# Kernel tuning notes

Hardware: AMD Instinct MI355X
Metric: run time of the kernel (lower is better)

The kernel has to match this reference:

```python
import jax, jax.numpy as jnp
import numpy as np

NUM_STEPS = 32
SEQ = 64
IN = 512
HID = 256
NUM_CLASSES = 10
BATCH = 2048


def _lstm_layer(xseq, Wih, Whh, bih, bhh):
    # xseq: (T, B, D). PyTorch LSTMCell gate order: i, f, g, o.
    B = xseq.shape[1]
    H = Whh.shape[1]
    h0 = jnp.zeros((B, H), xseq.dtype)
    c0 = jnp.zeros((B, H), xseq.dtype)
    b = bih + bhh

    def step(carry, x):
        h, c = carry
        gates = x @ Wih.T + h @ Whh.T + b  # (B, 4H)
        i, f, g, o = jnp.split(gates, 4, axis=-1)
        c_new = jax.nn.sigmoid(f) * c + jax.nn.sigmoid(i) * jnp.tanh(g)
        h_new = jax.nn.sigmoid(o) * jnp.tanh(c_new)
        return (h_new, c_new), h_new

    (hT, cT), hs = jax.lax.scan(step, (h0, c0), xseq)
    return hs, hT


def _run_stack(xseq, layer_params):
    hT = None
    for (Wih, Whh, bih, bhh) in layer_params:
        xseq, hT = _lstm_layer(xseq, Wih, Whh, bih, bhh)
    return hT


def setup_inputs() -> dict:
    key = jax.random.key(0)
    ks = jax.random.split(key, 32)
    d = {"xs": jax.random.normal(ks[0], (BATCH, SEQ, IN), dtype=jnp.float32)}
    cfg = [IN, HID, HID]
    ki = 1
    for direc in ("f", "r"):
        for l, (di, dh) in enumerate(zip(cfg[:-1], cfg[1:])):
            s = 1.0 / np.sqrt(dh)
            d[f"Wih_{direc}{l}"] = jax.random.uniform(ks[ki], (4 * dh, di), minval=-s, maxval=s); ki += 1
            d[f"Whh_{direc}{l}"] = jax.random.uniform(ks[ki], (4 * dh, dh), minval=-s, maxval=s); ki += 1
            d[f"bih_{direc}{l}"] = jax.random.uniform(ks[ki], (4 * dh,), minval=-s, maxval=s); ki += 1
            d[f"bhh_{direc}{l}"] = jax.random.uniform(ks[ki], (4 * dh,), minval=-s, maxval=s); ki += 1
    s = 1.0 / np.sqrt(2 * HID)
    d["W3"] = jax.random.uniform(ks[ki], (NUM_CLASSES, 2 * HID), minval=-s, maxval=s); ki += 1
    d["b3"] = jax.random.uniform(ks[ki], (NUM_CLASSES,), minval=-s, maxval=s)
    return d


def reference(xs, Wih_f0, Whh_f0, bih_f0, bhh_f0, Wih_f1, Whh_f1, bih_f1, bhh_f1,
              Wih_r0, Whh_r0, bih_r0, bhh_r0, Wih_r1, Whh_r1, bih_r1, bhh_r1, W3, b3):
    # forward direction: timesteps 62-NUM_STEPS .. 61
    xf = jnp.transpose(xs[:, 62 - NUM_STEPS:62, :], (1, 0, 2))  # (T, B, D)
    hF = _run_stack(xf, [(Wih_f0, Whh_f0, bih_f0, bhh_f0),
                         (Wih_f1, Whh_f1, bih_f1, bhh_f1)])
    # reverse direction: last 3 frames in order 63, 62, 61
    xr = jnp.transpose(jnp.flip(xs[:, 61:64, :], axis=1), (1, 0, 2))  # (3, B, D)
    hR = _run_stack(xr, [(Wih_r0, Whh_r0, bih_r0, bhh_r0),
                         (Wih_r1, Whh_r1, bih_r1, bhh_r1)])
    latent = jnp.concatenate([hF, hR], axis=1)  # (B, 512)
    return latent @ W3.T + b3
```

## Files before the change

### kernel.cpp

```cpp
#include <hip/hip_runtime.h>
#include <stdint.h>

typedef unsigned short u16;
typedef unsigned long long u64;
typedef __attribute__((ext_vector_type(8)))  short  bf16x8;
typedef __attribute__((ext_vector_type(8)))  u16    u16x8;
typedef __attribute__((ext_vector_type(4)))  float  f32x4;
typedef __attribute__((ext_vector_type(16))) _Float16 f16x16;

#define MFMA_BF16(a,b,c) __builtin_amdgcn_mfma_f32_16x16x32_bf16((a),(b),(c),0,0,0)

#define BATCH   2048
#define FSTEPS  32
#define RSTEPS  3
#define NVF     35

static constexpr size_t HROW32 = 128;
static constexpr size_t HPAR32 = (size_t)BATCH * HROW32;

static constexpr size_t OFF_CTL  = 0;
static constexpr size_t OFF_H0G  = 32768;
static constexpr size_t OFF_H1G  = OFF_H0G + HPAR32 * 2 * 4;
static constexpr size_t OFF_LAT  = OFF_H1G + HPAR32 * 2 * 4;
static constexpr size_t OFF_XP   = OFF_LAT + (size_t)BATCH * 512 * 4;
static constexpr size_t XP_BYTES = (size_t)NVF * BATCH * 1024 * 2;
static constexpr size_t OFF_W0XF = OFF_XP + XP_BYTES;
static constexpr size_t OFF_W0XR = OFF_W0XF + (size_t)1024 * 512 * 2;
static constexpr size_t OFF_P0F  = OFF_W0XR + (size_t)1024 * 512 * 2;
static constexpr size_t OFF_P0R  = OFF_P0F + (size_t)32768 * 16;
static constexpr size_t OFF_P1F  = OFF_P0R + (size_t)32768 * 16;
static constexpr size_t OFF_P1R  = OFF_P1F + (size_t)65536 * 16;
static constexpr size_t OFF_BS0F = OFF_P1R + (size_t)65536 * 16;
static constexpr size_t OFF_BS0R = OFF_BS0F + 4096;
static constexpr size_t OFF_BS1F = OFF_BS0R + 4096;
static constexpr size_t OFF_BS1R = OFF_BS1F + 4096;
static constexpr size_t WS_NEED  = OFF_BS1R + 4096;

__device__ __forceinline__ u16 f2bf(float f) {
    unsigned u = __float_as_uint(f);
    unsigned r = (u + 0x7fffu + ((u >> 16) & 1u)) >> 16;
    return (u16)r;
}
__device__ __forceinline__ float sigm(float x) { return 1.0f / (1.0f + __expf(-x)); }
__device__ __forceinline__ float tanh_fast(float x) {
    float a = fabsf(x);
    float e = __expf(-2.0f * a);
    float t = (1.0f - e) / (1.0f + e);
    return x < 0.0f ? -t : t;
}
__device__ __forceinline__ u16 f2h(float f) {
    _Float16 h = (_Float16)f;
    union { _Float16 h; u16 b; } u; u.h = h; return u.b;
}

__device__ __forceinline__ bf16x8 ldsA(const char* H, int row, int k) {
    int byte = (row << 9) + (k << 1);
    byte ^= (row & 7) << 4;
    return *(const bf16x8*)(H + byte);
}

__device__ __forceinline__ void reload32(char* Hs, const u64* src, int rg, int tid) {
    u64 v[8];
#pragma unroll
    for (int i = 0; i < 8; ++i) {
        int idx = tid + (i << 8);
        v[i] = __hip_atomic_load(src + ((size_t)rg * 32 + (idx >> 6)) * 64 + (idx & 63),
                                 __ATOMIC_RELAXED, __HIP_MEMORY_SCOPE_AGENT);
    }
#pragma unroll
    for (int i = 0; i < 8; ++i) {
        int idx = tid + (i << 8);
        int row = idx >> 6, cu = idx & 63;
        int byte = (row << 9) + (cu << 3);
        byte ^= (row & 7) << 4;
        *(u64*)(Hs + byte) = v[i];
    }
}

__global__ void __launch_bounds__(256)
lstm_seq(const _Float16* __restrict__ xp,
         const u16* __restrict__ P0f_, const u16* __restrict__ P0r_,
         const u16* __restrict__ P1f_, const u16* __restrict__ P1r_,
         const float* __restrict__ bs1f, const float* __restrict__ bs1r,
         unsigned* __restrict__ h0g, unsigned* __restrict__ h1g,
         float* __restrict__ latent, unsigned* __restrict__ ctl)
{
    __shared__ char T0[16384];
    __shared__ char T1[16384];
    const int tid = threadIdx.x, wq = tid >> 6, lane = tid & 63;
    const int bid = blockIdx.x;
    const int colq = bid >> 6;
    const int rg   = bid & 63;
    const int mem  = colq * 4 + wq;
    const int hc   = mem * 16 + (lane & 15);
    const int klane = lane >> 4, q4 = klane << 2;
    unsigned* flag = ctl + (size_t)rg * 64;
    unsigned bcount = 0;

    for (int dir = 0; dir < 2; ++dir) {
        const int nst = dir ? RSTEPS : FSTEPS;
        const int gbase = dir ? FSTEPS : 0;
        const bf16x8* P0v = (const bf16x8*)(dir ? P0r_ : P0f_) + (size_t)mem * (8 * 4 * 64);
        const bf16x8* P1v = (const bf16x8*)(dir ? P1r_ : P1f_) + (size_t)mem * (16 * 4 * 64);
        const float* bs1 = dir ? bs1r : bs1f;
        float b1reg[4];
#pragma unroll
        for (int g = 0; g < 4; ++g) b1reg[g] = bs1[g * 256 + hc];

        float c0[2][4], c1[2][4];
#pragma unroll
        for (int Mt = 0; Mt < 2; ++Mt)
#pragma unroll
            for (int r = 0; r < 4; ++r) { c0[Mt][r] = 0.f; c1[Mt][r] = 0.f; }

        __syncthreads();
#pragma unroll
        for (int i = 0; i < 4; ++i) {
            ((f32x4*)T0)[i * 256 + tid] = (f32x4){0.f, 0.f, 0.f, 0.f};
            ((f32x4*)T1)[i * 256 + tid] = (f32x4){0.f, 0.f, 0.f, 0.f};
        }
        __syncthreads();

        f16x16 xqm[2];
#pragma unroll
        for (int Mt = 0; Mt < 2; ++Mt)
            xqm[Mt] = *(const f16x16*)(xp +
                ((((size_t)gbase * 128 + rg * 2 + Mt) * 16 + mem) * 64 + lane) * 16);

        for (int t = 0; t <= nst; ++t) {
            f32x4 acc1[4][2];
            if (t >= 1) {
#pragma unroll
                for (int g = 0; g < 4; ++g) { acc1[g][0] = (f32x4){0.f,0.f,0.f,0.f}; acc1[g][1] = (f32x4){0.f,0.f,0.f,0.f}; }
#pragma unroll
                for (int kc = 0; kc < 8; ++kc) {
                    bf16x8 a0 = ldsA(T0, (lane & 15),       kc * 32 + klane * 8);
                    bf16x8 a1 = ldsA(T0, 16 + (lane & 15),  kc * 32 + klane * 8);
#pragma unroll
                    for (int g = 0; g < 4; ++g) {
                        bf16x8 b = P1v[(kc * 4 + g) * 64 + lane];
                        acc1[g][0] = MFMA_BF16(a0, b, acc1[g][0]);
                        acc1[g][1] = MFMA_BF16(a1, b, acc1[g][1]);
                    }
                }
                if (t >= 2) {
#pragma unroll
                    for (int kc = 0; kc < 8; ++kc) {
                        bf16x8 a0 = ldsA(T1, (lane & 15),      kc * 32 + klane * 8);
                        bf16x8 a1 = ldsA(T1, 16 + (lane & 15), kc * 32 + klane * 8);
#pragma unroll
                        for (int g = 0; g < 4; ++g) {
                            bf16x8 b = P1v[((kc + 8) * 4 + g) * 64 + lane];
                            acc1[g][0] = MFMA_BF16(a0, b, acc1[g][0]);
                            acc1[g][1] = MFMA_BF16(a1, b, acc1[g][1]);
                        }
                    }
                }
            }

            f32x4 acc0[4][2];
            if (t < nst) {
#pragma unroll
                for (int g = 0; g < 4; ++g) { acc0[g][0] = (f32x4){0.f,0.f,0.f,0.f}; acc0[g][1] = (f32x4){0.f,0.f,0.f,0.f}; }
                if (t >= 1) {
#pragma unroll
                    for (int kc = 0; kc < 8; ++kc) {
                        bf16x8 a0 = ldsA(T0, (lane & 15),      kc * 32 + klane * 8);
                        bf16x8 a1 = ldsA(T0, 16 + (lane & 15), kc * 32 + klane * 8);
#pragma unroll
                        for (int g = 0; g < 4; ++g) {
                            bf16x8 b = P0v[(kc * 4 + g) * 64 + lane];
                            acc0[g][0] = MFMA_BF16(a0, b, acc0[g][0]);
                            acc0[g][1] = MFMA_BF16(a1, b, acc0[g][1]);
                        }
                    }
                }
            }

            if (t < nst) {
                unsigned* dst = h0g + (size_t)(t & 1) * HPAR32;
                const int cp = mem * 8 + ((lane & 15) >> 1);
#pragma unroll
                for (int Mt = 0; Mt < 2; ++Mt) {
                    float hn[4];
#pragma unroll
                    for (int r = 0; r < 4; ++r) {
                        float gi = acc0[0][Mt][r] + (float)xqm[Mt][0 * 4 + r];
                        float gf = acc0[1][Mt][r] + (float)xqm[Mt][1 * 4 + r];
                        float gg = acc0[2][Mt][r] + (float)xqm[Mt][2 * 4 + r];
                        float go = acc0[3][Mt][r] + (float)xqm[Mt][3 * 4 + r];
                        float cn = sigm(gf) * c0[Mt][r] + sigm(gi) * tanh_fast(gg);
                        c0[Mt][r] = cn;
                        hn[r] = sigm(go) * tanh_fast(cn);
                    }
                    const int rowbase = rg * 32 + Mt * 16 + q4;
#pragma unroll
                    for (int r = 0; r < 4; ++r) {
                        float p = __shfl_xor(hn[r], 1);
                        if (!(lane & 1)) {
                            unsigned w = (unsigned)f2bf(hn[r]) | ((unsigned)f2bf(p) << 16);
                            __hip_atomic_store(dst + (size_t)(rowbase + r) * HROW32 + cp, w,
                                               __ATOMIC_RELAXED, __HIP_MEMORY_SCOPE_AGENT);
                        }
                    }
                }
            }

            if (t >= 1) {
                const int cp = mem * 8 + ((lane & 15) >> 1);
#pragma unroll
                for (int Mt = 0; Mt < 2; ++Mt) {
                    float hn[4];
#pragma unroll
                    for (int r = 0; r < 4; ++r) {
                        float gi = acc1[0][Mt][r] + b1reg[0];
                        float gf = acc1[1][Mt][r] + b1reg[1];
                        float gg = acc1[2][Mt][r] + b1reg[2];
                        float go = acc1[3][Mt][r] + b1reg[3];
                        float cn = sigm(gf) * c1[Mt][r] + sigm(gi) * tanh_fast(gg);
                        c1[Mt][r] = cn;
                        hn[r] = sigm(go) * tanh_fast(cn);
                    }
                    const int rowbase = rg * 32 + Mt * 16 + q4;
                    if (t < nst) {
                        unsigned* dst = h1g + (size_t)((t - 1) & 1) * HPAR32;
#pragma unroll
                        for (int r = 0; r < 4; ++r) {
                            float p = __shfl_xor(hn[r], 1);
                            if (!(lane & 1)) {
                                unsigned w = (unsigned)f2bf(hn[r]) | ((unsigned)f2bf(p) << 16);
                                __hip_atomic_store(dst + (size_t)(rowbase + r) * HROW32 + cp, w,
                                                   __ATOMIC_RELAXED, __HIP_MEMORY_SCOPE_AGENT);
                            }
                        }
                    } else {
#pragma unroll
                        for (int r = 0; r < 4; ++r)
                            latent[(size_t)(rowbase + r) * 512 + dir * 256 + hc] = hn[r];
                    }
                }
            }

            if (t < nst) {
                ++bcount;
                asm volatile("s_waitcnt vmcnt(0)" ::: "memory");
                __syncthreads();
                if (tid == 0)
                    __hip_atomic_fetch_add(flag, 1u, __ATOMIC_RELAXED, __HIP_MEMORY_SCOPE_AGENT);
                if (t + 1 < nst) {
#pragma unroll
                    for (int Mt = 0; Mt < 2; ++Mt)
                        xqm[Mt] = *(const f16x16*)(xp +
                            ((((size_t)(gbase + t + 1) * 128 + rg * 2 + Mt) * 16 + mem) * 64 + lane) * 16);
                }
                if (tid == 0) {
                    while (__hip_atomic_load(flag, __ATOMIC_RELAXED, __HIP_MEMORY_SCOPE_AGENT)
                           < 4u * bcount) {}
                }
                __syncthreads();
                __builtin_amdgcn_sched_barrier(0);
                reload32(T0, (const u64*)(h0g + (size_t)(t & 1) * HPAR32), rg, tid);
                if (t >= 1)
                    reload32(T1, (const u64*)(h1g + (size_t)((t - 1) & 1) * HPAR32), rg, tid);
                __syncthreads();
            }
        }
    }
}

__global__ void __launch_bounds__(256)
xproj_gemm(const float* __restrict__ xs,
           const u16* __restrict__ W0xf, const u16* __restrict__ W0xr,
           const float* __restrict__ bs0f, const float* __restrict__ bs0r,
           _Float16* __restrict__ xp)
{
    __shared__ char As[16384];
    __shared__ char Bs[16384];
    const int tid = threadIdx.x, wv = tid >> 6, lane = tid & 63;
    const int phys = blockIdx.x;
    const int xcd = phys & 7, idx = phys >> 3;
    const int mt = xcd * 70 + (idx >> 3);
    const int nt = idx & 7;
    const int vf = mt >> 4;
    const int dirr = (vf >= 32);
    const int frame = dirr ? (95 - vf) : (30 + vf);
    const int brow = (mt & 15) * 128;
    const u16* Wp = (dirr ? W0xr : W0xf) + (size_t)nt * 128 * 512;
    const float* bs = dirr ? bs0r : bs0f;

    float breg[8];
#pragma unroll
    for (int n = 0; n < 8; ++n) breg[n] = bs[nt * 128 + n * 16 + (lane & 15)];

    f32x4 acc[8][2];
#pragma unroll
    for (int n = 0; n < 8; ++n) { acc[n][0] = (f32x4){0.f,0.f,0.f,0.f}; acc[n][1] = (f32x4){0.f,0.f,0.f,0.f}; }

    const int ar = tid >> 1, akoff = (tid & 1) * 32;
    const float* asrc0 = xs + ((size_t)(brow + ar) * 64 + frame) * 512 + akoff;

    for (int c = 0; c < 8; ++c) {
        {
            const float* s = asrc0 + c * 64;
            u16x8 o[4];
#pragma unroll
            for (int j2 = 0; j2 < 4; ++j2) {
                float4 f0 = *(const float4*)(s + j2 * 8);
                float4 f1 = *(const float4*)(s + j2 * 8 + 4);
                u16x8 o_;
                o_[0] = f2bf(f0.x); o_[1] = f2bf(f0.y); o_[2] = f2bf(f0.z); o_[3] = f2bf(f0.w);
                o_[4] = f2bf(f1.x); o_[5] = f2bf(f1.y); o_[6] = f2bf(f1.z); o_[7] = f2bf(f1.w);
                o[j2] = o_;
            }
#pragma unroll
            for (int j2 = 0; j2 < 4; ++j2) {
                int k = akoff + j2 * 8;
                int byte = (ar << 7) + (k << 1); byte ^= (ar & 7) << 4;
                *(u16x8*)(As + byte) = o[j2];
            }
        }
#pragma unroll
        for (int i = 0; i < 4; ++i) {
            int u = tid + i * 256;
            int ns = u >> 3, c8 = (u & 7) << 3;
            u16x8 v = *(const u16x8*)(Wp + (size_t)ns * 512 + c * 64 + c8);
            int byte = (ns << 7) + (c8 << 1); byte ^= (ns & 7) << 4;
            *(u16x8*)(Bs + byte) = v;
        }
        __syncthreads();
#pragma unroll
        for (int kk = 0; kk < 2; ++kk) {
            int kin = kk * 32 + (lane >> 4) * 8;
            bf16x8 a0, a1;
            int row = wv * 32 + (lane & 15);
            int byte = (row << 7) + (kin << 1); byte ^= (row & 7) << 4;
            a0 = *(const bf16x8*)(As + byte);
            int row1 = row + 16;
            byte = (row1 << 7) + (kin << 1); byte ^= (row1 & 7) << 4;
            a1 = *(const bf16x8*)(As + byte);
#pragma unroll
            for (int n = 0; n < 8; ++n) {
                int ns = n * 16 + (lane & 15);
                int bb = (ns << 7) + (kin << 1); bb ^= (ns & 7) << 4;
                bf16x8 bf_ = *(const bf16x8*)(Bs + bb);
                acc[n][0] = MFMA_BF16(a0, bf_, acc[n][0]);
                acc[n][1] = MFMA_BF16(a1, bf_, acc[n][1]);
            }
        }
        __syncthreads();
    }
#pragma unroll
    for (int n = 0; n < 8; ++n)
#pragma unroll
        for (int mm = 0; mm < 2; ++mm) {
            u64 pk = 0;
#pragma unroll
            for (int r = 0; r < 4; ++r)
                pk |= (u64)f2h(acc[n][mm][r] + breg[n]) << (16 * r);
            int vm  = mt * 128 + wv * 32 + mm * 16 + ((lane >> 4) << 2);
            int col = nt * 128 + n * 16 + (lane & 15);
            int vf2 = vm >> 11, brow2 = vm & 2047;
            int rb2 = brow2 >> 4, sub = brow2 & 15;
            int lane2 = ((sub >> 2) << 4) + (col & 15);
            int m2 = (col >> 4) & 15, g2 = col >> 8;
            size_t o = ((((size_t)vf2 * 128 + rb2) * 16 + m2) * 64 + lane2) * 16 + (g2 << 2);
            *(u64*)(xp + o) = pk;
        }
}

__global__ void pack_w(const float* __restrict__ Wa, int da,
                       const float* __restrict__ bi, const float* __restrict__ bh,
                       u16* __restrict__ Wout, float* __restrict__ bout)
{
    int total = 1024 * da;
    int gt = blockIdx.x * blockDim.x + threadIdx.x;
    int stride = gridDim.x * blockDim.x;
    for (int i = gt; i < total; i += stride) Wout[i] = f2bf(Wa[i]);
    if (bout && gt < 1024) bout[gt] = bi[gt] + bh[gt];
}

__global__ void pack_frag(const float* __restrict__ Wa, int da,
                          const float* __restrict__ Wb, int db,
                          int nkc, u16* __restrict__ out,
                          const float* __restrict__ bi, const float* __restrict__ bh,
                          float* __restrict__ bout)
{
    int total = 16 * nkc * 4 * 64;
    int gt = blockIdx.x * blockDim.x + threadIdx.x;
    int stride = gridDim.x * blockDim.x;
    for (int u = gt; u < total; u += stride) {
        int l = u & 63;
        int t1 = u >> 6;
        int g = t1 & 3;
        int t2 = t1 >> 2;
        int kc = t2 % nkc;
        int mem = t2 / nkc;
        int row = g * 256 + mem * 16 + (l & 15);
        int k0 = kc * 32 + ((l >> 4) << 3);
        u16x8 o;
#pragma unroll
        for (int jj = 0; jj < 8; ++jj) {
            int k = k0 + jj;
            float v = (k < da) ? Wa[(size_t)row * da + k] : Wb[(size_t)row * db + (k - da)];
            o[jj] = f2bf(v);
        }
        *(u16x8*)(out + (size_t)u * 8) = o;
    }
    if (bout && gt < 1024) bout[gt] = bi[gt] + bh[gt];
}

__global__ void final_linear(const float* __restrict__ latent, const float* __restrict__ W3,
                             const float* __restrict__ b3, float* __restrict__ out)
{
    int idx = blockIdx.x * blockDim.x + threadIdx.x;
    if (idx >= BATCH * 10) return;
    int bb = idx / 10, c = idx - bb * 10;
    const float* lrow = latent + (size_t)bb * 512;
    const float* wrow = W3 + (size_t)c * 512;
    float s = b3[c];
#pragma unroll 4
    for (int k = 0; k < 512; k += 4) {
        float4 lv = *(const float4*)(lrow + k);
        float4 wv = *(const float4*)(wrow + k);
        s += lv.x * wv.x + lv.y * wv.y + lv.z * wv.z + lv.w * wv.w;
    }
    out[idx] = s;
}

extern "C" void kernel_launch(void* const* d_in, const int* in_sizes, int n_in,
                              void* d_out, int out_size, void* d_ws, size_t ws_size,
                              hipStream_t stream)
{
    (void)in_sizes; (void)n_in; (void)out_size;
    if (ws_size < WS_NEED) return;

    const float* xs     = (const float*)d_in[0];
    const float* Wih_f0 = (const float*)d_in[1];
    const float* Whh_f0 = (const float*)d_in[2];
    const float* bih_f0 = (const float*)d_in[3];
    const float* bhh_f0 = (const float*)d_in[4];
    const float* Wih_f1 = (const float*)d_in[5];
    const float* Whh_f1 = (const float*)d_in[6];
    const float* bih_f1 = (const float*)d_in[7];
    const float* bhh_f1 = (const float*)d_in[8];
    const float* Wih_r0 = (const float*)d_in[9];
    const float* Whh_r0 = (const float*)d_in[10];
    const float* bih_r0 = (const float*)d_in[11];
    const float* bhh_r0 = (const float*)d_in[12];
    const float* Wih_r1 = (const float*)d_in[13];
    const float* Whh_r1 = (const float*)d_in[14];
    const float* bih_r1 = (const float*)d_in[15];
    const float* bhh_r1 = (const float*)d_in[16];
    const float* W3     = (const float*)d_in[17];
    const float* b3     = (const float*)d_in[18];

    char* ws = (char*)d_ws;
    unsigned* ctl = (unsigned*)(ws + OFF_CTL);
    unsigned* h0g = (unsigned*)(ws + OFF_H0G);
    unsigned* h1g = (unsigned*)(ws + OFF_H1G);
    float* latent = (float*)(ws + OFF_LAT);
    _Float16* xp  = (_Float16*)(ws + OFF_XP);
    u16* W0xf = (u16*)(ws + OFF_W0XF);
    u16* W0xr = (u16*)(ws + OFF_W0XR);
    u16* P0f  = (u16*)(ws + OFF_P0F);
    u16* P0r  = (u16*)(ws + OFF_P0R);
    u16* P1f  = (u16*)(ws + OFF_P1F);
    u16* P1r  = (u16*)(ws + OFF_P1R);
    float* bs0f = (float*)(ws + OFF_BS0F);
    float* bs0r = (float*)(ws + OFF_BS0R);
    float* bs1f = (float*)(ws + OFF_BS1F);
    float* bs1r = (float*)(ws + OFF_BS1R);

    hipMemsetAsync(ctl, 0, 32768, stream);

    pack_w<<<256, 256, 0, stream>>>(Wih_f0, 512, bih_f0, bhh_f0, W0xf, bs0f);
    pack_w<<<256, 256, 0, stream>>>(Wih_r0, 512, bih_r0, bhh_r0, W0xr, bs0r);
    pack_frag<<<64, 256, 0, stream>>>(Whh_f0, 256, Whh_f0, 0, 8,  P0f, nullptr, nullptr, nullptr);
    pack_frag<<<64, 256, 0, stream>>>(Whh_r0, 256, Whh_r0, 0, 8,  P0r, nullptr, nullptr, nullptr);
    pack_frag<<<64, 256, 0, stream>>>(Wih_f1, 256, Whh_f1, 256, 16, P1f, bih_f1, bhh_f1, bs1f);
    pack_frag<<<64, 256, 0, stream>>>(Wih_r1, 256, Whh_r1, 256, 16, P1r, bih_r1, bhh_r1, bs1r);

    xproj_gemm<<<4480, 256, 0, stream>>>(xs, W0xf, W0xr, bs0f, bs0r, xp);

    lstm_seq<<<256, 256, 0, stream>>>(xp, P0f, P0r, P1f, P1r, bs1f, bs1r,
                                      h0g, h1g, latent, ctl);

    final_linear<<<80, 256, 0, stream>>>(latent, W3, b3, (float*)d_out);
}
```

Measured before the change: 867.8 us.

## Run reverse-direction LSTM stack concurrently with forward steps in one loop

Merges the separate forward and reverse direction loops into a single timestep loop. The 3-step reverse stack now runs inside the first forward iterations and shares their grid-wide barriers. This removes the reverse direction's own barriers and serial steps, which sat on the critical path. In exchange the kernel needs separate hidden-state buffers and double the LDS (64KB per block), adds extra reloads and MFMA work in the early steps, and raises register pressure.

After: 947.2 us. 9.1% more time.

```diff
diff --git a/kernel.cpp b/kernel.cpp
--- a/kernel.cpp
+++ b/kernel.cpp
@@ -21,7 +21,9 @@
 static constexpr size_t OFF_CTL  = 0;
 static constexpr size_t OFF_H0G  = 32768;
 static constexpr size_t OFF_H1G  = OFF_H0G + HPAR32 * 2 * 4;
-static constexpr size_t OFF_LAT  = OFF_H1G + HPAR32 * 2 * 4;
+static constexpr size_t OFF_H0GR = OFF_H1G + HPAR32 * 2 * 4;
+static constexpr size_t OFF_H1GR = OFF_H0GR + HPAR32 * 2 * 4;
+static constexpr size_t OFF_LAT  = OFF_H1GR + HPAR32 * 2 * 4;
 static constexpr size_t OFF_XP   = OFF_LAT + (size_t)BATCH * 512 * 4;
 static constexpr size_t XP_BYTES = (size_t)NVF * BATCH * 1024 * 2;
 static constexpr size_t OFF_W0XF = OFF_XP + XP_BYTES;
@@ -83,10 +85,13 @@
          const u16* __restrict__ P1f_, const u16* __restrict__ P1r_,
          const float* __restrict__ bs1f, const float* __restrict__ bs1r,
          unsigned* __restrict__ h0g, unsigned* __restrict__ h1g,
+         unsigned* __restrict__ h0gr, unsigned* __restrict__ h1gr,
          float* __restrict__ latent, unsigned* __restrict__ ctl)
 {
     __shared__ char T0[16384];
     __shared__ char T1[16384];
+    __shared__ char T0r[16384];
+    __shared__ char T1r[16384];
     const int tid = threadIdx.x, wq = tid >> 6, lane = tid & 63;
     const int bid = blockIdx.x;
     const int colq = bid >> 6;
@@ -94,106 +99,138 @@
     const int mem  = colq * 4 + wq;
     const int hc   = mem * 16 + (lane & 15);
     const int klane = lane >> 4, q4 = klane << 2;
+    const int cp   = mem * 8 + ((lane & 15) >> 1);
     unsigned* flag = ctl + (size_t)rg * 64;
     unsigned bcount = 0;
 
-    for (int dir = 0; dir < 2; ++dir) {
-        const int nst = dir ? RSTEPS : FSTEPS;
-        const int gbase = dir ? FSTEPS : 0;
-        const bf16x8* P0v = (const bf16x8*)(dir ? P0r_ : P0f_) + (size_t)mem * (8 * 4 * 64);
-        const bf16x8* P1v = (const bf16x8*)(dir ? P1r_ : P1f_) + (size_t)mem * (16 * 4 * 64);
-        const float* bs1 = dir ? bs1r : bs1f;
-        float b1reg[4];
-#pragma unroll
-        for (int g = 0; g < 4; ++g) b1reg[g] = bs1[g * 256 + hc];
-
-        float c0[2][4], c1[2][4];
-#pragma unroll
-        for (int Mt = 0; Mt < 2; ++Mt)
-#pragma unroll
-            for (int r = 0; r < 4; ++r) { c0[Mt][r] = 0.f; c1[Mt][r] = 0.f; }
-
-        __syncthreads();
-#pragma unroll
-        for (int i = 0; i < 4; ++i) {
-            ((f32x4*)T0)[i * 256 + tid] = (f32x4){0.f, 0.f, 0.f, 0.f};
-            ((f32x4*)T1)[i * 256 + tid] = (f32x4){0.f, 0.f, 0.f, 0.f};
-        }
-        __syncthreads();
-
-        f16x16 xqm[2];
-#pragma unroll
-        for (int Mt = 0; Mt < 2; ++Mt)
-            xqm[Mt] = *(const f16x16*)(xp +
-                ((((size_t)gbase * 128 + rg * 2 + Mt) * 16 + mem) * 64 + lane) * 16);
-
-        for (int t = 0; t <= nst; ++t) {
-            f32x4 acc1[4][2];
-            if (t >= 1) {
-#pragma unroll
-                for (int g = 0; g < 4; ++g) { acc1[g][0] = (f32x4){0.f,0.f,0.f,0.f}; acc1[g][1] = (f32x4){0.f,0.f,0.f,0.f}; }
+    const bf16x8* P0vf = (const bf16x8*)P0f_ + (size_t)mem * (8 * 4 * 64);
+    const bf16x8* P0vr = (const bf16x8*)P0r_ + (size_t)mem * (8 * 4 * 64);
+    const bf16x8* P1vf = (const bf16x8*)P1f_ + (size_t)mem * (16 * 4 * 64);
+    const bf16x8* P1vr = (const bf16x8*)P1r_ + (size_t)mem * (16 * 4 * 64);
+    float b1f[4], b1r[4];
+#pragma unroll
+    for (int g = 0; g < 4; ++g) { b1f[g] = bs1f[g * 256 + hc]; b1r[g] = bs1r[g * 256 + hc]; }
+
+    float c0f[2][4], c1f[2][4], c0r[2][4], c1r[2][4];
+#pragma unroll
+    for (int Mt = 0; Mt < 2; ++Mt)
+#pragma unroll
+        for (int r = 0; r < 4; ++r) {
+            c0f[Mt][r] = 0.f; c1f[Mt][r] = 0.f; c0r[Mt][r] = 0.f; c1r[Mt][r] = 0.f;
+        }
+
+    __syncthreads();
+#pragma unroll
+    for (int i = 0; i < 4; ++i) {
+        ((f32x4*)T0)[i * 256 + tid]  = (f32x4){0.f, 0.f, 0.f, 0.f};
+        ((f32x4*)T1)[i * 256 + tid]  = (f32x4){0.f, 0.f, 0.f, 0.f};
+        ((f32x4*)T0r)[i * 256 + tid] = (f32x4){0.f, 0.f, 0.f, 0.f};
+        ((f32x4*)T1r)[i * 256 + tid] = (f32x4){0.f, 0.f, 0.f, 0.f};
+    }
+    __syncthreads();
+
+    f16x16 xqf[2], xqr[2];
+#pragma unroll
+    for (int Mt = 0; Mt < 2; ++Mt) {
+        xqf[Mt] = *(const f16x16*)(xp + ((((size_t)0  * 128 + rg * 2 + Mt) * 16 + mem) * 64 + lane) * 16);
+        xqr[Mt] = *(const f16x16*)(xp + ((((size_t)32 * 128 + rg * 2 + Mt) * 16 + mem) * 64 + lane) * 16);
+    }
+
+    for (int t = 0; t <= FSTEPS; ++t) {
+        f32x4 acc1[4][2];
+        if (t >= 1) {
+#pragma unroll
+            for (int g = 0; g < 4; ++g) { acc1[g][0] = (f32x4){0.f,0.f,0.f,0.f}; acc1[g][1] = (f32x4){0.f,0.f,0.f,0.f}; }
+#pragma unroll
+            for (int kc = 0; kc < 8; ++kc) {
+                bf16x8 a0 = ldsA(T0, (lane & 15),       kc * 32 + klane * 8);
+                bf16x8 a1 = ldsA(T0, 16 + (lane & 15),  kc * 32 + klane * 8);
+#pragma unroll
+                for (int g = 0; g < 4; ++g) {
+                    bf16x8 b = P1vf[(kc * 4 + g) * 64 + lane];
+                    acc1[g][0] = MFMA_BF16(a0, b, acc1[g][0]);
+                    acc1[g][1] = MFMA_BF16(a1, b, acc1[g][1]);
+                }
+            }
+            if (t >= 2) {
 #pragma unroll
                 for (int kc = 0; kc < 8; ++kc) {
-                    bf16x8 a0 = ldsA(T0, (lane & 15),       kc * 32 + klane * 8);
-                    bf16x8 a1 = ldsA(T0, 16 + (lane & 15),  kc * 32 + klane * 8);
+                    bf16x8 a0 = ldsA(T1, (lane & 15),      kc * 32 + klane * 8);
+                    bf16x8 a1 = ldsA(T1, 16 + (lane & 15), kc * 32 + klane * 8);
 #pragma unroll
                     for (int g = 0; g < 4; ++g) {
-                        bf16x8 b = P1v[(kc * 4 + g) * 64 + lane];
+                        bf16x8 b = P1vf[((kc + 8) * 4 + g) * 64 + lane];
                         acc1[g][0] = MFMA_BF16(a0, b, acc1[g][0]);
                         acc1[g][1] = MFMA_BF16(a1, b, acc1[g][1]);
                     }
                 }
-                if (t >= 2) {
-#pragma unroll
-                    for (int kc = 0; kc < 8; ++kc) {
-                        bf16x8 a0 = ldsA(T1, (lane & 15),      kc * 32 + klane * 8);
-                        bf16x8 a1 = ldsA(T1, 16 + (lane & 15), kc * 32 + klane * 8);
-#pragma unroll
-                        for (int g = 0; g < 4; ++g) {
-                            bf16x8 b = P1v[((kc + 8) * 4 + g) * 64 + lane];
-                            acc1[g][0] = MFMA_BF16(a0, b, acc1[g][0]);
-                            acc1[g][1] = MFMA_BF16(a1, b, acc1[g][1]);
-                        }
-                    }
-                }
-            }
-
-            f32x4 acc0[4][2];
-            if (t < nst) {
-#pragma unroll
-                for (int g = 0; g < 4; ++g) { acc0[g][0] = (f32x4){0.f,0.f,0.f,0.f}; acc0[g][1] = (f32x4){0.f,0.f,0.f,0.f}; }
-                if (t >= 1) {
-#pragma unroll
-                    for (int kc = 0; kc < 8; ++kc) {
-                        bf16x8 a0 = ldsA(T0, (lane & 15),      kc * 32 + klane * 8);
-                        bf16x8 a1 = ldsA(T0, 16 + (lane & 15), kc * 32 + klane * 8);
-#pragma unroll
-                        for (int g = 0; g < 4; ++g) {
-                            bf16x8 b = P0v[(kc * 4 + g) * 64 + lane];
-                            acc0[g][0] = MFMA_BF16(a0, b, acc0[g][0]);
-                            acc0[g][1] = MFMA_BF16(a1, b, acc0[g][1]);
-                        }
-                    }
-                }
-            }
-
-            if (t < nst) {
-                unsigned* dst = h0g + (size_t)(t & 1) * HPAR32;
-                const int cp = mem * 8 + ((lane & 15) >> 1);
-#pragma unroll
-                for (int Mt = 0; Mt < 2; ++Mt) {
-                    float hn[4];
-#pragma unroll
-                    for (int r = 0; r < 4; ++r) {
-                        float gi = acc0[0][Mt][r] + (float)xqm[Mt][0 * 4 + r];
-                        float gf = acc0[1][Mt][r] + (float)xqm[Mt][1 * 4 + r];
-                        float gg = acc0[2][Mt][r] + (float)xqm[Mt][2 * 4 + r];
-                        float go = acc0[3][Mt][r] + (float)xqm[Mt][3 * 4 + r];
-                        float cn = sigm(gf) * c0[Mt][r] + sigm(gi) * tanh_fast(gg);
-                        c0[Mt][r] = cn;
-                        hn[r] = sigm(go) * tanh_fast(cn);
-                    }
-                    const int rowbase = rg * 32 + Mt * 16 + q4;
+            }
+        }
+
+        f32x4 acc0[4][2];
+        if (t < FSTEPS) {
+#pragma unroll
+            for (int g = 0; g < 4; ++g) { acc0[g][0] = (f32x4){0.f,0.f,0.f,0.f}; acc0[g][1] = (f32x4){0.f,0.f,0.f,0.f}; }
+            if (t >= 1) {
+#pragma unroll
+                for (int kc = 0; kc < 8; ++kc) {
+                    bf16x8 a0 = ldsA(T0, (lane & 15),      kc * 32 + klane * 8);
+                    bf16x8 a1 = ldsA(T0, 16 + (lane & 15), kc * 32 + klane * 8);
+#pragma unroll
+                    for (int g = 0; g < 4; ++g) {
+                        bf16x8 b = P0vf[(kc * 4 + g) * 64 + lane];
+                        acc0[g][0] = MFMA_BF16(a0, b, acc0[g][0]);
+                        acc0[g][1] = MFMA_BF16(a1, b, acc0[g][1]);
+                    }
+                }
+            }
+        }
+
+        if (t < FSTEPS) {
+            unsigned* dst = h0g + (size_t)(t & 1) * HPAR32;
+#pragma unroll
+            for (int Mt = 0; Mt < 2; ++Mt) {
+                float hn[4];
+#pragma unroll
+                for (int r = 0; r < 4; ++r) {
+                    float gi = acc0[0][Mt][r] + (float)xqf[Mt][0 * 4 + r];
+                    float gf = acc0[1][Mt][r] + (float)xqf[Mt][1 * 4 + r];
+                    float gg = acc0[2][Mt][r] + (float)xqf[Mt][2 * 4 + r];
+                    float go = acc0[3][Mt][r] + (float)xqf[Mt][3 * 4 + r];
+                    float cn = sigm(gf) * c0f[Mt][r] + sigm(gi) * tanh_fast(gg);
+                    c0f[Mt][r] = cn;
+                    hn[r] = sigm(go) * tanh_fast(cn);
+                }
+                const int rowbase = rg * 32 + Mt * 16 + q4;
+#pragma unroll
+                for (int r = 0; r < 4; ++r) {
+                    float p = __shfl_xor(hn[r], 1);
+                    if (!(lane & 1)) {
+                        unsigned w = (unsigned)f2bf(hn[r]) | ((unsigned)f2bf(p) << 16);
+                        __hip_atomic_store(dst + (size_t)(rowbase + r) * HROW32 + cp, w,
+                                           __ATOMIC_RELAXED, __HIP_MEMORY_SCOPE_AGENT);
+                    }
+                }
+            }
+        }
+
+        if (t >= 1) {
+#pragma unroll
+            for (int Mt = 0; Mt < 2; ++Mt) {
+                float hn[4];
+#pragma unroll
+                for (int r = 0; r < 4; ++r) {
+                    float gi = acc1[0][Mt][r] + b1f[0];
+                    float gf = acc1[1][Mt][r] + b1f[1];
+                    float gg = acc1[2][Mt][r] + b1f[2];
+                    float go = acc1[3][Mt][r] + b1f[3];
+                    float cn = sigm(gf) * c1f[Mt][r] + sigm(gi) * tanh_fast(gg);
+                    c1f[Mt][r] = cn;
+                    hn[r] = sigm(go) * tanh_fast(cn);
+                }
+                const int rowbase = rg * 32 + Mt * 16 + q4;
+                if (t < FSTEPS) {
+                    unsigned* dst = h1g + (size_t)((t - 1) & 1) * HPAR32;
 #pragma unroll
                     for (int r = 0; r < 4; ++r) {
                         float p = __shfl_xor(hn[r], 1);
@@ -203,27 +240,59 @@
                                                __ATOMIC_RELAXED, __HIP_MEMORY_SCOPE_AGENT);
                         }
                     }
-                }
-            }
-
+                } else {
+#pragma unroll
+                    for (int r = 0; r < 4; ++r)
+                        latent[(size_t)(rowbase + r) * 512 + hc] = hn[r];
+                }
+            }
+        }
+
+        if (t <= 3) {
             if (t >= 1) {
-                const int cp = mem * 8 + ((lane & 15) >> 1);
+                f32x4 ar1[4][2];
+#pragma unroll
+                for (int g = 0; g < 4; ++g) { ar1[g][0] = (f32x4){0.f,0.f,0.f,0.f}; ar1[g][1] = (f32x4){0.f,0.f,0.f,0.f}; }
+#pragma unroll
+                for (int kc = 0; kc < 8; ++kc) {
+                    bf16x8 a0 = ldsA(T0r, (lane & 15),      kc * 32 + klane * 8);
+                    bf16x8 a1 = ldsA(T0r, 16 + (lane & 15), kc * 32 + klane * 8);
+#pragma unroll
+                    for (int g = 0; g < 4; ++g) {
+                        bf16x8 b = P1vr[(kc * 4 + g) * 64 + lane];
+                        ar1[g][0] = MFMA_BF16(a0, b, ar1[g][0]);
+                        ar1[g][1] = MFMA_BF16(a1, b, ar1[g][1]);
+                    }
+                }
+                if (t >= 2) {
+#pragma unroll
+                    for (int kc = 0; kc < 8; ++kc) {
+                        bf16x8 a0 = ldsA(T1r, (lane & 15),      kc * 32 + klane * 8);
+                        bf16x8 a1 = ldsA(T1r, 16 + (lane & 15), kc * 32 + klane * 8);
+#pragma unroll
+                        for (int g = 0; g < 4; ++g) {
+                            bf16x8 b = P1vr[((kc + 8) * 4 + g) * 64 + lane];
+                            ar1[g][0] = MFMA_BF16(a0, b, ar1[g][0]);
+                            ar1[g][1] = MFMA_BF16(a1, b, ar1[g][1]);
+                        }
+                    }
+                }
 #pragma unroll
                 for (int Mt = 0; Mt < 2; ++Mt) {
                     float hn[4];
 #pragma unroll
                     for (int r = 0; r < 4; ++r) {
-                        float gi = acc1[0][Mt][r] + b1reg[0];
-                        float gf = acc1[1][Mt][r] + b1reg[1];
-                        float gg = acc1[2][Mt][r] + b1reg[2];
-                        float go = acc1[3][Mt][r] + b1reg[3];
-                        float cn = sigm(gf) * c1[Mt][r] + sigm(gi) * tanh_fast(gg);
-                        c1[Mt][r] = cn;
+                        float gi = ar1[0][Mt][r] + b1r[0];
+                        float gf = ar1[1][Mt][r] + b1r[1];
+                        float gg = ar1[2][Mt][r] + b1r[2];
+                        float go = ar1[3][Mt][r] + b1r[3];
+                        float cn = sigm(gf) * c1r[Mt][r] + sigm(gi) * tanh_fast(gg);
+                        c1r[Mt][r] = cn;
                         hn[r] = sigm(go) * tanh_fast(cn);
                     }
                     const int rowbase = rg * 32 + Mt * 16 + q4;
-                    if (t < nst) {
-                        unsigned* dst = h1g + (size_t)((t - 1) & 1) * HPAR32;
+                    if (t < RSTEPS) {
+                        unsigned* dst = h1gr + (size_t)((t - 1) & 1) * HPAR32;
 #pragma unroll
                         for (int r = 0; r < 4; ++r) {
                             float p = __shfl_xor(hn[r], 1);
@@ -236,34 +305,88 @@
                     } else {
 #pragma unroll
                         for (int r = 0; r < 4; ++r)
-                            latent[(size_t)(rowbase + r) * 512 + dir * 256 + hc] = hn[r];
-                    }
-                }
-            }
-
-            if (t < nst) {
-                ++bcount;
-                asm volatile("s_waitcnt vmcnt(0)" ::: "memory");
-                __syncthreads();
-                if (tid == 0)
-                    __hip_atomic_fetch_add(flag, 1u, __ATOMIC_RELAXED, __HIP_MEMORY_SCOPE_AGENT);
-                if (t + 1 < nst) {
-#pragma unroll
-                    for (int Mt = 0; Mt < 2; ++Mt)
-                        xqm[Mt] = *(const f16x16*)(xp +
-                            ((((size_t)(gbase + t + 1) * 128 + rg * 2 + Mt) * 16 + mem) * 64 + lane) * 16);
-                }
-                if (tid == 0) {
-                    while (__hip_atomic_load(flag, __ATOMIC_RELAXED, __HIP_MEMORY_SCOPE_AGENT)
-                           < 4u * bcount) {}
-                }
-                __syncthreads();
-                __builtin_amdgcn_sched_barrier(0);
-                reload32(T0, (const u64*)(h0g + (size_t)(t & 1) * HPAR32), rg, tid);
-                if (t >= 1)
-                    reload32(T1, (const u64*)(h1g + (size_t)((t - 1) & 1) * HPAR32), rg, tid);
-                __syncthreads();
-            }
+                            latent[(size_t)(rowbase + r) * 512 + 256 + hc] = hn[r];
+                    }
+                }
+            }
+
+            if (t < RSTEPS) {
+                f32x4 ar0[4][2];
+#pragma unroll
+                for (int g = 0; g < 4; ++g) { ar0[g][0] = (f32x4){0.f,0.f,0.f,0.f}; ar0[g][1] = (f32x4){0.f,0.f,0.f,0.f}; }
+                if (t >= 1) {
+#pragma unroll
+                    for (int kc = 0; kc < 8; ++kc) {
+                        bf16x8 a0 = ldsA(T0r, (lane & 15),      kc * 32 + klane * 8);
+                        bf16x8 a1 = ldsA(T0r, 16 + (lane & 15), kc * 32 + klane * 8);
+#pragma unroll
+                        for (int g = 0; g < 4; ++g) {
+                            bf16x8 b = P0vr[(kc * 4 + g) * 64 + lane];
+                            ar0[g][0] = MFMA_BF16(a0, b, ar0[g][0]);
+                            ar0[g][1] = MFMA_BF16(a1, b, ar0[g][1]);
+                        }
+                    }
+                }
+                unsigned* dst = h0gr + (size_t)(t & 1) * HPAR32;
+#pragma unroll
+                for (int Mt = 0; Mt < 2; ++Mt) {
+                    float hn[4];
+#pragma unroll
+                    for (int r = 0; r < 4; ++r) {
+                        float gi = ar0[0][Mt][r] + (float)xqr[Mt][0 * 4 + r];
+                        float gf = ar0[1][Mt][r] + (float)xqr[Mt][1 * 4 + r];
+                        float gg = ar0[2][Mt][r] + (float)xqr[Mt][2 * 4 + r];
+                        float go = ar0[3][Mt][r] + (float)xqr[Mt][3 * 4 + r];
+                        float cn = sigm(gf) * c0r[Mt][r] + sigm(gi) * tanh_fast(gg);
+                        c0r[Mt][r] = cn;
+                        hn[r] = sigm(go) * tanh_fast(cn);
+                    }
+                    const int rowbase = rg * 32 + Mt * 16 + q4;
+#pragma unroll
+                    for (int r = 0; r < 4; ++r) {
+                        float p = __shfl_xor(hn[r], 1);
+                        if (!(lane & 1)) {
+                            unsigned w = (unsigned)f2bf(hn[r]) | ((unsigned)f2bf(p) << 16);
+                            __hip_atomic_store(dst + (size_t)(rowbase + r) * HROW32 + cp, w,
+                                               __ATOMIC_RELAXED, __HIP_MEMORY_SCOPE_AGENT);
+                        }
+                    }
+                }
+            }
+        }
+
+        if (t < FSTEPS) {
+            ++bcount;
+            asm volatile("s_waitcnt vmcnt(0)" ::: "memory");
+            __syncthreads();
+            if (tid == 0)
+                __hip_atomic_fetch_add(flag, 1u, __ATOMIC_RELAXED, __HIP_MEMORY_SCOPE_AGENT);
+            if (t + 1 < FSTEPS) {
+#pragma unroll
+                for (int Mt = 0; Mt < 2; ++Mt)
+                    xqf[Mt] = *(const f16x16*)(xp +
+                        ((((size_t)(t + 1) * 128 + rg * 2 + Mt) * 16 + mem) * 64 + lane) * 16);
+            }
+            if (t + 1 < RSTEPS) {
+#pragma unroll
+                for (int Mt = 0; Mt < 2; ++Mt)
+                    xqr[Mt] = *(const f16x16*)(xp +
+                        ((((size_t)(32 + t + 1) * 128 + rg * 2 + Mt) * 16 + mem) * 64 + lane) * 16);
+            }
+            if (tid == 0) {
+                while (__hip_atomic_load(flag, __ATOMIC_RELAXED, __HIP_MEMORY_SCOPE_AGENT)
+                       < 4u * bcount) {}
+            }
+            __syncthreads();
+            __builtin_amdgcn_sched_barrier(0);
+            reload32(T0, (const u64*)(h0g + (size_t)(t & 1) * HPAR32), rg, tid);
+            if (t >= 1)
+                reload32(T1, (const u64*)(h1g + (size_t)((t - 1) & 1) * HPAR32), rg, tid);
+            if (t < RSTEPS)
+                reload32(T0r, (const u64*)(h0gr + (size_t)(t & 1) * HPAR32), rg, tid);
+            if (t >= 1 && t < RSTEPS)
+                reload32(T1r, (const u64*)(h1gr + (size_t)((t - 1) & 1) * HPAR32), rg, tid);
+            __syncthreads();
         }
     }
 }
@@ -455,9 +578,11 @@
     const float* b3     = (const float*)d_in[18];
 
     char* ws = (char*)d_ws;
-    unsigned* ctl = (unsigned*)(ws + OFF_CTL);
-    unsigned* h0g = (unsigned*)(ws + OFF_H0G);
-    unsigned* h1g = (unsigned*)(ws + OFF_H1G);
+    unsigned* ctl  = (unsigned*)(ws + OFF_CTL);
+    unsigned* h0g  = (unsigned*)(ws + OFF_H0G);
+    unsigned* h1g  = (unsigned*)(ws + OFF_H1G);
+    unsigned* h0gr = (unsigned*)(ws + OFF_H0GR);
+    unsigned* h1gr = (unsigned*)(ws + OFF_H1GR);
     float* latent = (float*)(ws + OFF_LAT);
     _Float16* xp  = (_Float16*)(ws + OFF_XP);
     u16* W0xf = (u16*)(ws + OFF_W0XF);
@@ -483,7 +608,7 @@
     xproj_gemm<<<4480, 256, 0, stream>>>(xs, W0xf, W0xr, bs0f, bs0r, xp);
 
     lstm_seq<<<256, 256, 0, stream>>>(xp, P0f, P0r, P1f, P1r, bs1f, bs1r,
-                                      h0g, h1g, latent, ctl);
+                                      h0g, h1g, h0gr, h1gr, latent, ctl);
 
     final_linear<<<80, 256, 0, stream>>>(latent, W3, b3, (float*)d_out);
 }
```

## Restructure input projection GEMM to full-K LDS tile with pre-packed weight fragments

Applied to the files above, without the earlier changes.

The input-projection GEMM now has each block hold a 32-row, full-K (512) slice of x in LDS. Each wave computes a 256-column slab of all 1024 gate outputs, loading B operands directly from global memory in a pre-packed MFMA fragment layout made by pack_frag. The per-K-chunk LDS staging of both operands and its barriers go away, x is read and converted once per block, and the grid is halved. In exchange the kernel depends on cache-served global weight loads inside the MFMA loop and holds more accumulators per thread, which may lower occupancy.

Result: slower. 1.251 ms (+44.2%).

```diff
diff --git a/kernel.cpp b/kernel.cpp
--- a/kernel.cpp
+++ b/kernel.cpp
@@ -24,9 +24,9 @@
 static constexpr size_t OFF_LAT  = OFF_H1G + HPAR32 * 2 * 4;
 static constexpr size_t OFF_XP   = OFF_LAT + (size_t)BATCH * 512 * 4;
 static constexpr size_t XP_BYTES = (size_t)NVF * BATCH * 1024 * 2;
-static constexpr size_t OFF_W0XF = OFF_XP + XP_BYTES;
-static constexpr size_t OFF_W0XR = OFF_W0XF + (size_t)1024 * 512 * 2;
-static constexpr size_t OFF_P0F  = OFF_W0XR + (size_t)1024 * 512 * 2;
+static constexpr size_t OFF_P0XF = OFF_XP + XP_BYTES;
+static constexpr size_t OFF_P0XR = OFF_P0XF + (size_t)65536 * 16;
+static constexpr size_t OFF_P0F  = OFF_P0XR + (size_t)65536 * 16;
 static constexpr size_t OFF_P0R  = OFF_P0F + (size_t)32768 * 16;
 static constexpr size_t OFF_P1F  = OFF_P0R + (size_t)32768 * 16;
 static constexpr size_t OFF_P1R  = OFF_P1F + (size_t)65536 * 16;
@@ -57,6 +57,11 @@
     int byte = (row << 9) + (k << 1);
     byte ^= (row & 7) << 4;
     return *(const bf16x8*)(H + byte);
+}
+__device__ __forceinline__ bf16x8 ldsX(const char* X, int row, int k) {
+    int byte = (row << 10) + (k << 1);
+    byte ^= (row & 7) << 4;
+    return *(const bf16x8*)(X + byte);
 }
 
 __device__ __forceinline__ void reload32(char* Hs, const u64* src, int rg, int tid) {
@@ -270,113 +275,69 @@
 
 __global__ void __launch_bounds__(256)
 xproj_gemm(const float* __restrict__ xs,
-           const u16* __restrict__ W0xf, const u16* __restrict__ W0xr,
+           const u16* __restrict__ P0xf, const u16* __restrict__ P0xr,
            const float* __restrict__ bs0f, const float* __restrict__ bs0r,
            _Float16* __restrict__ xp)
 {
-    __shared__ char As[16384];
-    __shared__ char Bs[16384];
-    const int tid = threadIdx.x, wv = tid >> 6, lane = tid & 63;
-    const int phys = blockIdx.x;
-    const int xcd = phys & 7, idx = phys >> 3;
-    const int mt = xcd * 70 + (idx >> 3);
-    const int nt = idx & 7;
-    const int vf = mt >> 4;
+    __shared__ char X[32768];
+    const int tid = threadIdx.x, ws = tid >> 6, lane = tid & 63;
+    const int bid = blockIdx.x;
+    const int vf = bid >> 6;
+    const int rb = bid & 63;
     const int dirr = (vf >= 32);
     const int frame = dirr ? (95 - vf) : (30 + vf);
-    const int brow = (mt & 15) * 128;
-    const u16* Wp = (dirr ? W0xr : W0xf) + (size_t)nt * 128 * 512;
+    const bf16x8* Pv = (const bf16x8*)(dirr ? P0xr : P0xf);
     const float* bs = dirr ? bs0r : bs0f;
-
-    float breg[8];
-#pragma unroll
-    for (int n = 0; n < 8; ++n) breg[n] = bs[nt * 128 + n * 16 + (lane & 15)];
-
-    f32x4 acc[8][2];
-#pragma unroll
-    for (int n = 0; n < 8; ++n) { acc[n][0] = (f32x4){0.f,0.f,0.f,0.f}; acc[n][1] = (f32x4){0.f,0.f,0.f,0.f}; }
-
-    const int ar = tid >> 1, akoff = (tid & 1) * 32;
-    const float* asrc0 = xs + ((size_t)(brow + ar) * 64 + frame) * 512 + akoff;
-
-    for (int c = 0; c < 8; ++c) {
-        {
-            const float* s = asrc0 + c * 64;
-            u16x8 o[4];
-#pragma unroll
-            for (int j2 = 0; j2 < 4; ++j2) {
-                float4 f0 = *(const float4*)(s + j2 * 8);
-                float4 f1 = *(const float4*)(s + j2 * 8 + 4);
-                u16x8 o_;
-                o_[0] = f2bf(f0.x); o_[1] = f2bf(f0.y); o_[2] = f2bf(f0.z); o_[3] = f2bf(f0.w);
-                o_[4] = f2bf(f1.x); o_[5] = f2bf(f1.y); o_[6] = f2bf(f1.z); o_[7] = f2bf(f1.w);
-                o[j2] = o_;
-            }
-#pragma unroll
-            for (int j2 = 0; j2 < 4; ++j2) {
-                int k = akoff + j2 * 8;
-                int byte = (ar << 7) + (k << 1); byte ^= (ar & 7) << 4;
-                *(u16x8*)(As + byte) = o[j2];
-            }
+    const int klane = lane >> 4;
+
+#pragma unroll
+    for (int i = 0; i < 16; ++i) {
+        int u = tid + (i << 8);
+        int row = u >> 7, j = u & 127;
+        float4 v = *(const float4*)(xs + (((size_t)(rb * 32 + row) * 64 + frame) * 512 + j * 4));
+        u64 pk = (u64)f2bf(v.x) | ((u64)f2bf(v.y) << 16)
+               | ((u64)f2bf(v.z) << 32) | ((u64)f2bf(v.w) << 48);
+        int byte = (row << 10) + (j << 3);
+        byte ^= (row & 7) << 4;
+        *(u64*)(X + byte) = pk;
+    }
+    __syncthreads();
+
+    float breg[16];
+#pragma unroll
+    for (int nf = 0; nf < 16; ++nf) breg[nf] = bs[ws * 256 + nf * 16 + (lane & 15)];
+
+    f32x4 acc[2][16];
+#pragma unroll
+    for (int m = 0; m < 2; ++m)
+#pragma unroll
+        for (int nf = 0; nf < 16; ++nf) acc[m][nf] = (f32x4){0.f, 0.f, 0.f, 0.f};
+
+#pragma unroll 2
+    for (int kc = 0; kc < 16; ++kc) {
+        bf16x8 a0 = ldsX(X, (lane & 15),      kc * 32 + klane * 8);
+        bf16x8 a1 = ldsX(X, 16 + (lane & 15), kc * 32 + klane * 8);
+#pragma unroll
+        for (int nf = 0; nf < 16; ++nf) {
+            bf16x8 b = Pv[(size_t)nf * 4096 + (kc * 4 + ws) * 64 + lane];
+            acc[0][nf] = MFMA_BF16(a0, b, acc[0][nf]);
+            acc[1][nf] = MFMA_BF16(a1, b, acc[1][nf]);
         }
-#pragma unroll
-        for (int i = 0; i < 4; ++i) {
-            int u = tid + i * 256;
-            int ns = u >> 3, c8 = (u & 7) << 3;
-            u16x8 v = *(const u16x8*)(Wp + (size_t)ns * 512 + c * 64 + c8);
-            int byte = (ns << 7) + (c8 << 1); byte ^= (ns & 7) << 4;
-            *(u16x8*)(Bs + byte) = v;
-        }
-        __syncthreads();
-#pragma unroll
-        for (int kk = 0; kk < 2; ++kk) {
-            int kin = kk * 32 + (lane >> 4) * 8;
-            bf16x8 a0, a1;
-            int row = wv * 32 + (lane & 15);
-            int byte = (row << 7) + (kin << 1); byte ^= (row & 7) << 4;
-            a0 = *(const bf16x8*)(As + byte);
-            int row1 = row + 16;
-            byte = (row1 << 7) + (kin << 1); byte ^= (row1 & 7) << 4;
-            a1 = *(const bf16x8*)(As + byte);
-#pragma unroll
-            for (int n = 0; n < 8; ++n) {
-                int ns = n * 16 + (lane & 15);
-                int bb = (ns << 7) + (kin << 1); bb ^= (ns & 7) << 4;
-                bf16x8 bf_ = *(const bf16x8*)(Bs + bb);
-                acc[n][0] = MFMA_BF16(a0, bf_, acc[n][0]);
-                acc[n][1] = MFMA_BF16(a1, bf_, acc[n][1]);
-            }
-        }
-        __syncthreads();
-    }
-#pragma unroll
-    for (int n = 0; n < 8; ++n)
-#pragma unroll
-        for (int mm = 0; mm < 2; ++mm) {
+    }
+
+#pragma unroll
+    for (int m = 0; m < 2; ++m)
+#pragma unroll
+        for (int nf = 0; nf < 16; ++nf) {
             u64 pk = 0;
 #pragma unroll
             for (int r = 0; r < 4; ++r)
-                pk |= (u64)f2h(acc[n][mm][r] + breg[n]) << (16 * r);
-            int vm  = mt * 128 + wv * 32 + mm * 16 + ((lane >> 4) << 2);
-            int col = nt * 128 + n * 16 + (lane & 15);
-            int vf2 = vm >> 11, brow2 = vm & 2047;
-            int rb2 = brow2 >> 4, sub = brow2 & 15;
-            int lane2 = ((sub >> 2) << 4) + (col & 15);
-            int m2 = (col >> 4) & 15, g2 = col >> 8;
-            size_t o = ((((size_t)vf2 * 128 + rb2) * 16 + m2) * 64 + lane2) * 16 + (g2 << 2);
+                pk |= (u64)f2h(acc[m][nf][r] + breg[nf]) << (16 * r);
+            int lane2 = (klane << 4) + (lane & 15);
+            size_t o = ((((size_t)vf * 128 + rb * 2 + m) * 16 + nf) * 64 + lane2) * 16
+                       + (ws << 2);
             *(u64*)(xp + o) = pk;
         }
-}
-
-__global__ void pack_w(const float* __restrict__ Wa, int da,
-                       const float* __restrict__ bi, const float* __restrict__ bh,
-                       u16* __restrict__ Wout, float* __restrict__ bout)
-{
-    int total = 1024 * da;
-    int gt = blockIdx.x * blockDim.x + threadIdx.x;
-    int stride = gridDim.x * blockDim.x;
-    for (int i = gt; i < total; i += stride) Wout[i] = f2bf(Wa[i]);
-    if (bout && gt < 1024) bout[gt] = bi[gt] + bh[gt];
 }
 
 __global__ void pack_frag(const float* __restrict__ Wa, int da,
@@ -460,8 +421,8 @@
     unsigned* h1g = (unsigned*)(ws + OFF_H1G);
     float* latent = (float*)(ws + OFF_LAT);
     _Float16* xp  = (_Float16*)(ws + OFF_XP);
-    u16* W0xf = (u16*)(ws + OFF_W0XF);
-    u16* W0xr = (u16*)(ws + OFF_W0XR);
+    u16* P0xf = (u16*)(ws + OFF_P0XF);
+    u16* P0xr = (u16*)(ws + OFF_P0XR);
     u16* P0f  = (u16*)(ws + OFF_P0F);
     u16* P0r  = (u16*)(ws + OFF_P0R);
     u16* P1f  = (u16*)(ws + OFF_P1F);
@@ -473,14 +434,14 @@
 
     hipMemsetAsync(ctl, 0, 32768, stream);
 
-    pack_w<<<256, 256, 0, stream>>>(Wih_f0, 512, bih_f0, bhh_f0, W0xf, bs0f);
-    pack_w<<<256, 256, 0, stream>>>(Wih_r0, 512, bih_r0, bhh_r0, W0xr, bs0r);
+    pack_frag<<<64, 256, 0, stream>>>(Wih_f0, 512, Wih_f0, 0, 16, P0xf, bih_f0, bhh_f0, bs0f);
+    pack_frag<<<64, 256, 0, stream>>>(Wih_r0, 512, Wih_r0, 0, 16, P0xr, bih_r0, bhh_r0, bs0r);
     pack_frag<<<64, 256, 0, stream>>>(Whh_f0, 256, Whh_f0, 0, 8,  P0f, nullptr, nullptr, nullptr);
     pack_frag<<<64, 256, 0, stream>>>(Whh_r0, 256, Whh_r0, 0, 8,  P0r, nullptr, nullptr, nullptr);
     pack_frag<<<64, 256, 0, stream>>>(Wih_f1, 256, Whh_f1, 256, 16, P1f, bih_f1, bhh_f1, bs1f);
     pack_frag<<<64, 256, 0, stream>>>(Wih_r1, 256, Whh_r1, 256, 16, P1r, bih_r1, bhh_r1, bs1r);
 
-    xproj_gemm<<<4480, 256, 0, stream>>>(xs, W0xf, W0xr, bs0f, bs0r, xp);
+    xproj_gemm<<<2240, 256, 0, stream>>>(xs, P0xf, P0xr, bs0f, bs0r, xp);
 
     lstm_seq<<<256, 256, 0, stream>>>(xp, P0f, P0r, P1f, P1r, bs1f, bs1r,
                                       h0g, h1g, latent, ctl);
```
